# Optimization experiments

Measured on AMD Instinct MI355X. Metric: run time of the kernel, lower is better.

The kernel has to match this reference:

```python
import jax, jax.numpy as jnp
import numpy as np

HIDDEN = 512
BATCH = 32
SEQ = 4096


def setup_inputs() -> dict:
    key = jax.random.key(0)
    ks = jax.random.split(key, 8)
    s = 1.0 / np.sqrt(HIDDEN)
    return {
        "encoder_outputs": jax.random.normal(ks[0], (BATCH, SEQ, HIDDEN), jnp.float32),
        "decoder_hidden": jax.random.normal(ks[1], (BATCH, HIDDEN), jnp.float32),
        "W_enc": jax.random.uniform(ks[2], (HIDDEN, HIDDEN), jnp.float32, -s, s),
        "b_enc": jax.random.uniform(ks[3], (HIDDEN,), jnp.float32, -s, s),
        "W_dec": jax.random.uniform(ks[4], (HIDDEN, HIDDEN), jnp.float32, -s, s),
        "b_dec": jax.random.uniform(ks[5], (HIDDEN,), jnp.float32, -s, s),
        "W_v": jax.random.uniform(ks[6], (HIDDEN, 1), jnp.float32, -s, s),
        "b_v": jax.random.uniform(ks[7], (1,), jnp.float32, -s, s),
    }


def reference(encoder_outputs, decoder_hidden, W_enc, b_enc, W_dec, b_dec, W_v, b_v):
    # (b, s, h) projected encoder states
    enc_proj = jnp.einsum("bsh,hk->bsk", encoder_outputs, W_enc) + b_enc
    # (b, 1, h) projected decoder state, broadcast-added over seq
    dec_proj = (decoder_hidden @ W_dec + b_dec)[:, None, :]
    # score: (b, s, 1)
    score = jnp.tanh(enc_proj + dec_proj) @ W_v + b_v
    attention_weights = jax.nn.softmax(score, axis=1)  # softmax over seq_len
    # context: (b, h) weighted sum of encoder outputs
    context = jnp.sum(attention_weights * encoder_outputs, axis=1)
    return context, jnp.squeeze(attention_weights, -1)
```

## Files before the change

### kernel.cpp

```cpp
#include <hip/hip_runtime.h>
#include <hip/hip_bf16.h>

typedef __attribute__((ext_vector_type(8))) short bf16x8;
typedef __attribute__((ext_vector_type(4))) float f32x4;

#define HID 512
#define NB 32
#define SEQL 4096
#define BM 64
#define NKC 16
#define NBLK 2048
#define APAD 8
#define AW (HID + APAD)

#define WS_BP    0
#define WS_DPROJ (512*1024)
#define WS_SUM   (576*1024)

__device__ __forceinline__ short f2bf(float f) {
    unsigned u = __float_as_uint(f);
    unsigned r = (u + 0x7fffu + ((u >> 16) & 1u)) >> 16;
    return (short)r;
}

__device__ __forceinline__ float fast_tanh(float x) {
    float e = __expf(2.0f * x);
    float r = __builtin_amdgcn_rcpf(e + 1.0f);
    return 1.0f - 2.0f * r;
}

__global__ void k_pre(const float* __restrict__ We, short* __restrict__ Bp,
                      const float* __restrict__ dec, const float* __restrict__ Wd,
                      const float* __restrict__ be, const float* __restrict__ bd,
                      float* __restrict__ dproj, float* __restrict__ out,
                      float* __restrict__ sumacc) {
    const int blk = blockIdx.x, t = threadIdx.x;
    if (blk < 128) {
        int tid  = blk * 256 + t;
        int lane = tid & 63;
        int nt   = (tid >> 6) & 31;
        int kc   = tid >> 11;
        int k0   = kc * 32 + (lane >> 4) * 8;
        int n    = nt * 16 + (lane & 15);
        bf16x8 v;
#pragma unroll
        for (int j = 0; j < 8; ++j) v[j] = f2bf(We[(size_t)(k0 + j) * HID + n]);
        *(bf16x8*)&Bp[(size_t)tid * 8] = v;
    } else if (blk < 640) {
        __shared__ float red[8][33];
        int bid2 = blk - 128;
        int b  = bid2 >> 4, kg = bid2 & 15;
        int kl = t & 31,    hc = t >> 5;
        int k  = kg * 32 + kl;
        const float* dr = dec + (size_t)b * HID;
        float a = 0.f;
#pragma unroll 8
        for (int j = 0; j < 64; ++j) {
            int h = hc * 64 + j;
            a += dr[h] * Wd[(size_t)h * HID + k];
        }
        red[hc][kl] = a;
        __syncthreads();
        if (hc == 0) {
            float s = be[k] + bd[k];
#pragma unroll
            for (int c = 0; c < 8; ++c) s += red[c][kl];
            dproj[(size_t)b * HID + k] = s;
        }
    } else {
        int bz = blk - 640;
        out[bz * 256 + t] = 0.f;
        if (bz == 0 && t < NB) sumacc[t] = 0.f;
    }
}

__global__ __launch_bounds__(256, 2)
void k_main(const float* __restrict__ E, const short* __restrict__ Bp,
            const float* __restrict__ dproj, const float* __restrict__ Wv,
            float* __restrict__ out, float* __restrict__ sumacc) {
    __shared__ short As[BM][AW];
    __shared__ float fbuf[640];
    __shared__ float pbuf[BM];

    const int tid  = threadIdx.x;
    const int wave = tid >> 6, lane = tid & 63;
    const int quad = lane >> 4, l15 = lane & 15;
    const int bid  = blockIdx.x;
    const int row0 = bid * BM;
    const int b    = bid >> 6;

    f32x4 acc[4][8];
#pragma unroll
    for (int r = 0; r < 4; ++r)
#pragma unroll
        for (int c = 0; c < 8; ++c) acc[r][c] = (f32x4){0.f, 0.f, 0.f, 0.f};

    const float4* E4 = (const float4*)E + (size_t)row0 * (HID / 4);
    const int drow = tid >> 7;
    const int dcol = (tid & 127) * 4;
#pragma unroll
    for (int ph = 0; ph < 4; ++ph) {
        float4 v[8];
#pragma unroll
        for (int j = 0; j < 8; ++j)
            v[j] = E4[(size_t)(ph * 8 + j) * 256 + tid];
#pragma unroll
        for (int j = 0; j < 8; ++j) {
            int row = (ph * 8 + j) * 2 + drow;
            short4 s;
            s.x = f2bf(v[j].x); s.y = f2bf(v[j].y);
            s.z = f2bf(v[j].z); s.w = f2bf(v[j].w);
            *(short4*)&As[row][dcol] = s;
        }
    }

    const short* bbase = Bp + ((size_t)(wave * 8) * 64 + lane) * 8;
    bf16x8 fb[2][4][2];
    bf16x8 fbr[2][8];
#pragma unroll
    for (int c = 0; c < 8; ++c)
        fbr[0][c] = *(const bf16x8*)(bbase + (size_t)c * 64 * 8);

    __syncthreads();

    bf16x8 fa[2][4];
#pragma unroll
    for (int r = 0; r < 4; ++r)
        fa[0][r] = *(const bf16x8*)&As[r * 16 + l15][quad * 8];

#pragma unroll
    for (int kc = 0; kc < NKC; ++kc) {
        const int cur = kc & 1, nxt = cur ^ 1;
        if (kc + 1 < NKC) {
#pragma unroll
            for (int c = 0; c < 8; ++c)
                fbr[nxt][c] = *(const bf16x8*)(bbase + ((size_t)(kc + 1) * 2048 + c * 64) * 8);
#pragma unroll
            for (int r = 0; r < 4; ++r)
                fa[nxt][r] = *(const bf16x8*)&As[r * 16 + l15][(kc + 1) * 32 + quad * 8];
        }
#pragma unroll
        for (int c = 0; c < 8; ++c)
#pragma unroll
            for (int r = 0; r < 4; ++r)
                acc[r][c] = __builtin_amdgcn_mfma_f32_16x16x32_bf16(fa[cur][r], fbr[cur][c], acc[r][c], 0, 0, 0);
    }

    float part[4][4];
#pragma unroll
    for (int r = 0; r < 4; ++r)
#pragma unroll
        for (int g = 0; g < 4; ++g) part[r][g] = 0.f;
    const float* dp = dproj + (size_t)b * HID;
#pragma unroll
    for (int c = 0; c < 8; ++c) {
        int col = wave * 128 + c * 16 + l15;
        float dv = dp[col];
        float wv = Wv[col];
#pragma unroll
        for (int r = 0; r < 4; ++r)
#pragma unroll
            for (int g = 0; g < 4; ++g)
                part[r][g] += fast_tanh(acc[r][c][g] + dv) * wv;
    }
#pragma unroll
    for (int r = 0; r < 4; ++r)
#pragma unroll
        for (int g = 0; g < 4; ++g) {
            float v = part[r][g];
            v += __shfl_xor(v, 1); v += __shfl_xor(v, 2);
            v += __shfl_xor(v, 4); v += __shfl_xor(v, 8);
            part[r][g] = v;
        }
    if (l15 == 0) {
#pragma unroll
        for (int r = 0; r < 4; ++r)
#pragma unroll
            for (int g = 0; g < 4; ++g)
                fbuf[wave * 64 + r * 16 + quad * 4 + g] = part[r][g];
    }
    __syncthreads();
    if (tid < 64) {
        float s  = fbuf[tid] + fbuf[64 + tid] + fbuf[128 + tid] + fbuf[192 + tid];
        float pv = __expf(s);
        pbuf[tid] = pv;
        out[(size_t)NB * HID + row0 + tid] = pv;
        float t2 = pv;
        t2 += __shfl_xor(t2, 1);  t2 += __shfl_xor(t2, 2);  t2 += __shfl_xor(t2, 4);
        t2 += __shfl_xor(t2, 8);  t2 += __shfl_xor(t2, 16); t2 += __shfl_xor(t2, 32);
        if (tid == 0) atomicAdd(&sumacc[b], t2);
    }
    __syncthreads();

    const int hq = tid & 127, rh = tid >> 7;
    const float4* Eb = (const float4*)E;
    size_t cbase = (size_t)(row0 + rh * 32) * (HID / 4) + hq;
    float4 ca = {0.f, 0.f, 0.f, 0.f};
#pragma unroll 4
    for (int rr = 0; rr < 32; ++rr) {
        float w  = pbuf[rh * 32 + rr];
        float4 e = Eb[cbase + (size_t)rr * (HID / 4)];
        ca.x += w * e.x; ca.y += w * e.y; ca.z += w * e.z; ca.w += w * e.w;
    }
    if (rh == 1) {
        fbuf[hq] = ca.x; fbuf[128 + hq] = ca.y; fbuf[256 + hq] = ca.z; fbuf[384 + hq] = ca.w;
    }
    __syncthreads();
    if (rh == 0) {
        ca.x += fbuf[hq]; ca.y += fbuf[128 + hq]; ca.z += fbuf[256 + hq]; ca.w += fbuf[384 + hq];
        float* cg = out + (size_t)b * HID + hq * 4;
        atomicAdd(cg + 0, ca.x); atomicAdd(cg + 1, ca.y);
        atomicAdd(cg + 2, ca.z); atomicAdd(cg + 3, ca.w);
    }
}

__global__ void k_finish(float* __restrict__ out, const float* __restrict__ sumacc) {
    int b = blockIdx.x, t = threadIdx.x;
    float rs = 1.0f / sumacc[b];
    for (int i = t; i < HID; i += 256)
        out[(size_t)b * HID + i] *= rs;
    float* ow = out + (size_t)NB * HID + (size_t)b * SEQL;
    for (int i = t; i < SEQL; i += 256)
        ow[i] *= rs;
}

extern "C" void kernel_launch(void* const* d_in, const int* in_sizes, int n_in,
                              void* d_out, int out_size, void* d_ws, size_t ws_size,
                              hipStream_t stream) {
    const float* E   = (const float*)d_in[0];
    const float* dec = (const float*)d_in[1];
    const float* We  = (const float*)d_in[2];
    const float* be  = (const float*)d_in[3];
    const float* Wd  = (const float*)d_in[4];
    const float* bd  = (const float*)d_in[5];
    const float* Wv  = (const float*)d_in[6];
    float* out = (float*)d_out;
    char*  ws  = (char*)d_ws;
    short* Bp     = (short*)(ws + WS_BP);
    float* dproj  = (float*)(ws + WS_DPROJ);
    float* sumacc = (float*)(ws + WS_SUM);

    k_pre<<<704, 256, 0, stream>>>(We, Bp, dec, Wd, be, bd, dproj, out, sumacc);
    k_main<<<NBLK, 256, 0, stream>>>(E, Bp, dproj, Wv, out, sumacc);
    k_finish<<<NB, 256, 0, stream>>>(out, sumacc);
}
```

Measured before the change: 492.5 us.

## Give each wave its own 16 rows, drop LDS staging, and replace atomics with partial buffers

The main kernel now has each wave own 16 encoder rows. A operands are loaded straight from global memory into registers as bf16, with no LDS staging. The kernel loops over 32-column groups, streaming the B fragments from global memory/L2, and occupancy is raised to 4 blocks. Context and exp-sum partials are written per block to workspace, and the finish kernel reduces them in place of float atomics, so the zero-init pass goes away. The trade-off is that B-fragment reuse across rows drops: each wave re-reads all of W_enc, which adds L2 traffic in exchange for higher occupancy and no atomics.

```diff
diff --git a/kernel.cpp b/kernel.cpp
--- a/kernel.cpp
+++ b/kernel.cpp
@@ -7,15 +7,13 @@
 #define HID 512
 #define NB 32
 #define SEQL 4096
-#define BM 64
 #define NKC 16
 #define NBLK 2048
-#define APAD 8
-#define AW (HID + APAD)
 
 #define WS_BP    0
 #define WS_DPROJ (512*1024)
-#define WS_SUM   (576*1024)
+#define WS_PC    (576*1024)
+#define WS_PCS   (576*1024 + 4*1024*1024)
 
 __device__ __forceinline__ short f2bf(float f) {
     unsigned u = __float_as_uint(f);
@@ -32,8 +30,7 @@
 __global__ void k_pre(const float* __restrict__ We, short* __restrict__ Bp,
                       const float* __restrict__ dec, const float* __restrict__ Wd,
                       const float* __restrict__ be, const float* __restrict__ bd,
-                      float* __restrict__ dproj, float* __restrict__ out,
-                      float* __restrict__ sumacc) {
+                      float* __restrict__ dproj) {
     const int blk = blockIdx.x, t = threadIdx.x;
     if (blk < 128) {
         int tid  = blk * 256 + t;
@@ -46,7 +43,7 @@
 #pragma unroll
         for (int j = 0; j < 8; ++j) v[j] = f2bf(We[(size_t)(k0 + j) * HID + n]);
         *(bf16x8*)&Bp[(size_t)tid * 8] = v;
-    } else if (blk < 640) {
+    } else {
         __shared__ float red[8][33];
         int bid2 = blk - 128;
         int b  = bid2 >> 4, kg = bid2 & 15;
@@ -67,158 +64,135 @@
             for (int c = 0; c < 8; ++c) s += red[c][kl];
             dproj[(size_t)b * HID + k] = s;
         }
-    } else {
-        int bz = blk - 640;
-        out[bz * 256 + t] = 0.f;
-        if (bz == 0 && t < NB) sumacc[t] = 0.f;
-    }
-}
-
-__global__ __launch_bounds__(256, 2)
+    }
+}
+
+__global__ __launch_bounds__(256, 4)
 void k_main(const float* __restrict__ E, const short* __restrict__ Bp,
             const float* __restrict__ dproj, const float* __restrict__ Wv,
-            float* __restrict__ out, float* __restrict__ sumacc) {
-    __shared__ short As[BM][AW];
-    __shared__ float fbuf[640];
-    __shared__ float pbuf[BM];
+            float* __restrict__ outw, float* __restrict__ pc,
+            float* __restrict__ pcs) {
+    __shared__ float ctxs[4][HID];
+    __shared__ float ssum[4];
 
     const int tid  = threadIdx.x;
     const int wave = tid >> 6, lane = tid & 63;
     const int quad = lane >> 4, l15 = lane & 15;
     const int bid  = blockIdx.x;
-    const int row0 = bid * BM;
+    const int row0 = bid * 64 + wave * 16;
     const int b    = bid >> 6;
 
-    f32x4 acc[4][8];
-#pragma unroll
-    for (int r = 0; r < 4; ++r)
-#pragma unroll
-        for (int c = 0; c < 8; ++c) acc[r][c] = (f32x4){0.f, 0.f, 0.f, 0.f};
-
-    const float4* E4 = (const float4*)E + (size_t)row0 * (HID / 4);
-    const int drow = tid >> 7;
-    const int dcol = (tid & 127) * 4;
-#pragma unroll
-    for (int ph = 0; ph < 4; ++ph) {
-        float4 v[8];
-#pragma unroll
-        for (int j = 0; j < 8; ++j)
-            v[j] = E4[(size_t)(ph * 8 + j) * 256 + tid];
-#pragma unroll
-        for (int j = 0; j < 8; ++j) {
-            int row = (ph * 8 + j) * 2 + drow;
-            short4 s;
-            s.x = f2bf(v[j].x); s.y = f2bf(v[j].y);
-            s.z = f2bf(v[j].z); s.w = f2bf(v[j].w);
-            *(short4*)&As[row][dcol] = s;
-        }
-    }
-
-    const short* bbase = Bp + ((size_t)(wave * 8) * 64 + lane) * 8;
-    bf16x8 fb[2][4][2];
-    bf16x8 fbr[2][8];
-#pragma unroll
-    for (int c = 0; c < 8; ++c)
-        fbr[0][c] = *(const bf16x8*)(bbase + (size_t)c * 64 * 8);
-
+    const float* ap = E + (size_t)(row0 + l15) * HID + quad * 8;
+    bf16x8 fa[NKC];
+#pragma unroll
+    for (int kc = 0; kc < NKC; ++kc) {
+        float4 a0 = *(const float4*)(ap + kc * 32);
+        float4 a1 = *(const float4*)(ap + kc * 32 + 4);
+        bf16x8 v;
+        v[0] = f2bf(a0.x); v[1] = f2bf(a0.y); v[2] = f2bf(a0.z); v[3] = f2bf(a0.w);
+        v[4] = f2bf(a1.x); v[5] = f2bf(a1.y); v[6] = f2bf(a1.z); v[7] = f2bf(a1.w);
+        fa[kc] = v;
+    }
+
+    const short* bbl = Bp + (size_t)lane * 8;
+    const float* dp  = dproj + (size_t)b * HID;
+    float sp[4] = {0.f, 0.f, 0.f, 0.f};
+
+    for (int cg = 0; cg < 16; ++cg) {
+        f32x4 a0 = (f32x4){0.f, 0.f, 0.f, 0.f};
+        f32x4 a1 = (f32x4){0.f, 0.f, 0.f, 0.f};
+        const short* bcg = bbl + (size_t)(cg * 2) * 512;
+#pragma unroll
+        for (int kc = 0; kc < NKC; ++kc) {
+            bf16x8 fb0 = *(const bf16x8*)(bcg + (size_t)kc * 16384);
+            bf16x8 fb1 = *(const bf16x8*)(bcg + (size_t)kc * 16384 + 512);
+            a0 = __builtin_amdgcn_mfma_f32_16x16x32_bf16(fa[kc], fb0, a0, 0, 0, 0);
+            a1 = __builtin_amdgcn_mfma_f32_16x16x32_bf16(fa[kc], fb1, a1, 0, 0, 0);
+        }
+        int c0 = cg * 32 + l15;
+        float dv0 = dp[c0],      wv0 = Wv[c0];
+        float dv1 = dp[c0 + 16], wv1 = Wv[c0 + 16];
+#pragma unroll
+        for (int g = 0; g < 4; ++g) {
+            sp[g] += fast_tanh(a0[g] + dv0) * wv0;
+            sp[g] += fast_tanh(a1[g] + dv1) * wv1;
+        }
+    }
+
+#pragma unroll
+    for (int g = 0; g < 4; ++g) {
+        float v = sp[g];
+        v += __shfl_xor(v, 1); v += __shfl_xor(v, 2);
+        v += __shfl_xor(v, 4); v += __shfl_xor(v, 8);
+        sp[g] = v;
+    }
+    float pv[4];
+#pragma unroll
+    for (int g = 0; g < 4; ++g) pv[g] = __expf(sp[g]);
+    if (l15 == 0) {
+#pragma unroll
+        for (int g = 0; g < 4; ++g) outw[row0 + quad * 4 + g] = pv[g];
+    }
+    float ws = pv[0] + pv[1] + pv[2] + pv[3];
+    ws += __shfl_xor(ws, 16); ws += __shfl_xor(ws, 32);
+    if (lane == 0) ssum[wave] = ws;
+
+    float pvr[16];
+#pragma unroll
+    for (int r = 0; r < 16; ++r) pvr[r] = __shfl(pv[r & 3], (r >> 2) * 16);
+    const float* er = E + (size_t)row0 * HID + lane * 8;
+    f32x4 c0 = (f32x4){0.f, 0.f, 0.f, 0.f};
+    f32x4 c1 = (f32x4){0.f, 0.f, 0.f, 0.f};
+#pragma unroll
+    for (int r = 0; r < 16; ++r) {
+        float4 e0 = *(const float4*)(er + (size_t)r * HID);
+        float4 e1 = *(const float4*)(er + (size_t)r * HID + 4);
+        float w = pvr[r];
+        c0.x += w * e0.x; c0.y += w * e0.y; c0.z += w * e0.z; c0.w += w * e0.w;
+        c1.x += w * e1.x; c1.y += w * e1.y; c1.z += w * e1.z; c1.w += w * e1.w;
+    }
+    *(f32x4*)&ctxs[wave][lane * 8]     = c0;
+    *(f32x4*)&ctxs[wave][lane * 8 + 4] = c1;
     __syncthreads();
 
-    bf16x8 fa[2][4];
-#pragma unroll
-    for (int r = 0; r < 4; ++r)
-        fa[0][r] = *(const bf16x8*)&As[r * 16 + l15][quad * 8];
-
-#pragma unroll
-    for (int kc = 0; kc < NKC; ++kc) {
-        const int cur = kc & 1, nxt = cur ^ 1;
-        if (kc + 1 < NKC) {
-#pragma unroll
-            for (int c = 0; c < 8; ++c)
-                fbr[nxt][c] = *(const bf16x8*)(bbase + ((size_t)(kc + 1) * 2048 + c * 64) * 8);
-#pragma unroll
-            for (int r = 0; r < 4; ++r)
-                fa[nxt][r] = *(const bf16x8*)&As[r * 16 + l15][(kc + 1) * 32 + quad * 8];
-        }
-#pragma unroll
-        for (int c = 0; c < 8; ++c)
-#pragma unroll
-            for (int r = 0; r < 4; ++r)
-                acc[r][c] = __builtin_amdgcn_mfma_f32_16x16x32_bf16(fa[cur][r], fbr[cur][c], acc[r][c], 0, 0, 0);
-    }
-
-    float part[4][4];
-#pragma unroll
-    for (int r = 0; r < 4; ++r)
-#pragma unroll
-        for (int g = 0; g < 4; ++g) part[r][g] = 0.f;
-    const float* dp = dproj + (size_t)b * HID;
-#pragma unroll
-    for (int c = 0; c < 8; ++c) {
-        int col = wave * 128 + c * 16 + l15;
-        float dv = dp[col];
-        float wv = Wv[col];
-#pragma unroll
-        for (int r = 0; r < 4; ++r)
-#pragma unroll
-            for (int g = 0; g < 4; ++g)
-                part[r][g] += fast_tanh(acc[r][c][g] + dv) * wv;
-    }
-#pragma unroll
-    for (int r = 0; r < 4; ++r)
-#pragma unroll
-        for (int g = 0; g < 4; ++g) {
-            float v = part[r][g];
-            v += __shfl_xor(v, 1); v += __shfl_xor(v, 2);
-            v += __shfl_xor(v, 4); v += __shfl_xor(v, 8);
-            part[r][g] = v;
-        }
-    if (l15 == 0) {
-#pragma unroll
-        for (int r = 0; r < 4; ++r)
-#pragma unroll
-            for (int g = 0; g < 4; ++g)
-                fbuf[wave * 64 + r * 16 + quad * 4 + g] = part[r][g];
-    }
+    if (tid < 128) {
+        int h = tid * 4;
+        f32x4 s = *(f32x4*)&ctxs[0][h];
+        f32x4 s1 = *(f32x4*)&ctxs[1][h];
+        f32x4 s2 = *(f32x4*)&ctxs[2][h];
+        f32x4 s3 = *(f32x4*)&ctxs[3][h];
+        s.x += s1.x + s2.x + s3.x; s.y += s1.y + s2.y + s3.y;
+        s.z += s1.z + s2.z + s3.z; s.w += s1.w + s2.w + s3.w;
+        *(f32x4*)&pc[(size_t)bid * HID + h] = s;
+    }
+    if (tid == 0) pcs[bid] = ssum[0] + ssum[1] + ssum[2] + ssum[3];
+}
+
+__global__ void k_finish(float* __restrict__ out, const float* __restrict__ pc,
+                         const float* __restrict__ pcs) {
+    __shared__ float red[64];
+    const int b = blockIdx.x, t = threadIdx.x;
+    if (t < 64) red[t] = pcs[b * 64 + t];
     __syncthreads();
-    if (tid < 64) {
-        float s  = fbuf[tid] + fbuf[64 + tid] + fbuf[128 + tid] + fbuf[192 + tid];
-        float pv = __expf(s);
-        pbuf[tid] = pv;
-        out[(size_t)NB * HID + row0 + tid] = pv;
-        float t2 = pv;
-        t2 += __shfl_xor(t2, 1);  t2 += __shfl_xor(t2, 2);  t2 += __shfl_xor(t2, 4);
-        t2 += __shfl_xor(t2, 8);  t2 += __shfl_xor(t2, 16); t2 += __shfl_xor(t2, 32);
-        if (tid == 0) atomicAdd(&sumacc[b], t2);
+    if (t < 16) {
+        float s = red[t] + red[t + 16] + red[t + 32] + red[t + 48];
+        red[t] = s;
     }
     __syncthreads();
-
-    const int hq = tid & 127, rh = tid >> 7;
-    const float4* Eb = (const float4*)E;
-    size_t cbase = (size_t)(row0 + rh * 32) * (HID / 4) + hq;
-    float4 ca = {0.f, 0.f, 0.f, 0.f};
-#pragma unroll 4
-    for (int rr = 0; rr < 32; ++rr) {
-        float w  = pbuf[rh * 32 + rr];
-        float4 e = Eb[cbase + (size_t)rr * (HID / 4)];
-        ca.x += w * e.x; ca.y += w * e.y; ca.z += w * e.z; ca.w += w * e.w;
-    }
-    if (rh == 1) {
-        fbuf[hq] = ca.x; fbuf[128 + hq] = ca.y; fbuf[256 + hq] = ca.z; fbuf[384 + hq] = ca.w;
-    }
-    __syncthreads();
-    if (rh == 0) {
-        ca.x += fbuf[hq]; ca.y += fbuf[128 + hq]; ca.z += fbuf[256 + hq]; ca.w += fbuf[384 + hq];
-        float* cg = out + (size_t)b * HID + hq * 4;
-        atomicAdd(cg + 0, ca.x); atomicAdd(cg + 1, ca.y);
-        atomicAdd(cg + 2, ca.z); atomicAdd(cg + 3, ca.w);
-    }
-}
-
-__global__ void k_finish(float* __restrict__ out, const float* __restrict__ sumacc) {
-    int b = blockIdx.x, t = threadIdx.x;
-    float rs = 1.0f / sumacc[b];
-    for (int i = t; i < HID; i += 256)
-        out[(size_t)b * HID + i] *= rs;
+    float total = 0.f;
+#pragma unroll
+    for (int i = 0; i < 16; ++i) total += red[i];
+    float rs = 1.0f / total;
+
+    const float* pcb = pc + (size_t)b * 64 * HID;
+#pragma unroll
+    for (int hh = 0; hh < 2; ++hh) {
+        int h = t + hh * 256;
+        float a = 0.f;
+#pragma unroll 8
+        for (int w = 0; w < 64; ++w) a += pcb[(size_t)w * HID + h];
+        out[(size_t)b * HID + h] = a * rs;
+    }
     float* ow = out + (size_t)NB * HID + (size_t)b * SEQL;
     for (int i = t; i < SEQL; i += 256)
         ow[i] *= rs;
@@ -236,11 +210,13 @@
     const float* Wv  = (const float*)d_in[6];
     float* out = (float*)d_out;
     char*  ws  = (char*)d_ws;
-    short* Bp     = (short*)(ws + WS_BP);
-    float* dproj  = (float*)(ws + WS_DPROJ);
-    float* sumacc = (float*)(ws + WS_SUM);
-
-    k_pre<<<704, 256, 0, stream>>>(We, Bp, dec, Wd, be, bd, dproj, out, sumacc);
-    k_main<<<NBLK, 256, 0, stream>>>(E, Bp, dproj, Wv, out, sumacc);
-    k_finish<<<NB, 256, 0, stream>>>(out, sumacc);
-}
+    short* Bp    = (short*)(ws + WS_BP);
+    float* dproj = (float*)(ws + WS_DPROJ);
+    float* pc    = (float*)(ws + WS_PC);
+    float* pcs   = (float*)(ws + WS_PCS);
+    float* outw  = out + (size_t)NB * HID;
+
+    k_pre<<<640, 256, 0, stream>>>(We, Bp, dec, Wd, be, bd, dproj);
+    k_main<<<NBLK, 256, 0, stream>>>(E, Bp, dproj, Wv, outw, pc, pcs);
+    k_finish<<<NB, 256, 0, stream>>>(out, pc, pcs);
+}
```

New measurement: 572.4 us. +16.2%, slower.

## Halve row tile and chunk columns to cut registers and raise occupancy

Applied to the files above, without the earlier changes.

The main kernel now handles 32 sequence rows per block instead of 64, doubling the grid. The GEMM loop walks four column groups, each with a 2x2 accumulator tile, so the 128-register accumulator array shrinks to 16 registers; launch bounds ask for 4 blocks per CU. This should allow more waves to hide memory latency. In exchange, each block re-reads the full bf16 weight matrix over half as many rows, and the context stage issues twice as many atomics.

```diff
diff --git a/kernel.cpp b/kernel.cpp
--- a/kernel.cpp
+++ b/kernel.cpp
@@ -7,9 +7,9 @@
 #define HID 512
 #define NB 32
 #define SEQL 4096
-#define BM 64
 #define NKC 16
-#define NBLK 2048
+#define BMR 32
+#define NBLK 4096
 #define APAD 8
 #define AW (HID + APAD)
 
@@ -74,140 +74,130 @@
     }
 }
 
-__global__ __launch_bounds__(256, 2)
+__global__ __launch_bounds__(256, 4)
 void k_main(const float* __restrict__ E, const short* __restrict__ Bp,
             const float* __restrict__ dproj, const float* __restrict__ Wv,
             float* __restrict__ out, float* __restrict__ sumacc) {
-    __shared__ short As[BM][AW];
-    __shared__ float fbuf[640];
-    __shared__ float pbuf[BM];
+    __shared__ short As[BMR][AW];
+    __shared__ float sred[4][32];
+    __shared__ float pbuf[BMR];
+    __shared__ float cred[512];
 
     const int tid  = threadIdx.x;
     const int wave = tid >> 6, lane = tid & 63;
     const int quad = lane >> 4, l15 = lane & 15;
     const int bid  = blockIdx.x;
-    const int row0 = bid * BM;
-    const int b    = bid >> 6;
-
-    f32x4 acc[4][8];
-#pragma unroll
-    for (int r = 0; r < 4; ++r)
-#pragma unroll
-        for (int c = 0; c < 8; ++c) acc[r][c] = (f32x4){0.f, 0.f, 0.f, 0.f};
+    const int row0 = bid * BMR;
+    const int b    = bid >> 7;
 
     const float4* E4 = (const float4*)E + (size_t)row0 * (HID / 4);
-    const int drow = tid >> 7;
-    const int dcol = (tid & 127) * 4;
-#pragma unroll
-    for (int ph = 0; ph < 4; ++ph) {
-        float4 v[8];
-#pragma unroll
-        for (int j = 0; j < 8; ++j)
-            v[j] = E4[(size_t)(ph * 8 + j) * 256 + tid];
-#pragma unroll
-        for (int j = 0; j < 8; ++j) {
-            int row = (ph * 8 + j) * 2 + drow;
-            short4 s;
-            s.x = f2bf(v[j].x); s.y = f2bf(v[j].y);
-            s.z = f2bf(v[j].z); s.w = f2bf(v[j].w);
-            *(short4*)&As[row][dcol] = s;
-        }
-    }
-
-    const short* bbase = Bp + ((size_t)(wave * 8) * 64 + lane) * 8;
-    bf16x8 fb[2][4][2];
-    bf16x8 fbr[2][8];
-#pragma unroll
-    for (int c = 0; c < 8; ++c)
-        fbr[0][c] = *(const bf16x8*)(bbase + (size_t)c * 64 * 8);
-
-    __syncthreads();
-
-    bf16x8 fa[2][4];
-#pragma unroll
-    for (int r = 0; r < 4; ++r)
-        fa[0][r] = *(const bf16x8*)&As[r * 16 + l15][quad * 8];
-
-#pragma unroll
-    for (int kc = 0; kc < NKC; ++kc) {
-        const int cur = kc & 1, nxt = cur ^ 1;
-        if (kc + 1 < NKC) {
-#pragma unroll
-            for (int c = 0; c < 8; ++c)
-                fbr[nxt][c] = *(const bf16x8*)(bbase + ((size_t)(kc + 1) * 2048 + c * 64) * 8);
-#pragma unroll
-            for (int r = 0; r < 4; ++r)
-                fa[nxt][r] = *(const bf16x8*)&As[r * 16 + l15][(kc + 1) * 32 + quad * 8];
-        }
-#pragma unroll
-        for (int c = 0; c < 8; ++c)
-#pragma unroll
-            for (int r = 0; r < 4; ++r)
-                acc[r][c] = __builtin_amdgcn_mfma_f32_16x16x32_bf16(fa[cur][r], fbr[cur][c], acc[r][c], 0, 0, 0);
-    }
-
-    float part[4][4];
-#pragma unroll
-    for (int r = 0; r < 4; ++r)
-#pragma unroll
-        for (int g = 0; g < 4; ++g) part[r][g] = 0.f;
+#pragma unroll
+    for (int i = 0; i < 16; ++i) {
+        int f = i * 256 + tid;
+        float4 v = E4[f];
+        int row = f >> 7, c4 = f & 127;
+        short4 s;
+        s.x = f2bf(v.x); s.y = f2bf(v.y); s.z = f2bf(v.z); s.w = f2bf(v.w);
+        *(short4*)&As[row][c4 * 4] = s;
+    }
+    __syncthreads();
+
     const float* dp = dproj + (size_t)b * HID;
-#pragma unroll
-    for (int c = 0; c < 8; ++c) {
-        int col = wave * 128 + c * 16 + l15;
-        float dv = dp[col];
-        float wv = Wv[col];
-#pragma unroll
-        for (int r = 0; r < 4; ++r)
-#pragma unroll
-            for (int g = 0; g < 4; ++g)
-                part[r][g] += fast_tanh(acc[r][c][g] + dv) * wv;
-    }
-#pragma unroll
-    for (int r = 0; r < 4; ++r)
+    float sp[2][4] = {{0.f,0.f,0.f,0.f},{0.f,0.f,0.f,0.f}};
+
+#pragma unroll 1
+    for (int cg = 0; cg < 4; ++cg) {
+        const int ntb = wave * 8 + cg * 2;
+        const short* bcg = Bp + ((size_t)ntb * 64 + lane) * 8;
+        int col = wave * 128 + cg * 32 + l15;
+        float dv0 = dp[col],      wv0 = Wv[col];
+        float dv1 = dp[col + 16], wv1 = Wv[col + 16];
+
+        f32x4 acc[2][2];
+#pragma unroll
+        for (int rt = 0; rt < 2; ++rt)
+#pragma unroll
+            for (int ct = 0; ct < 2; ++ct) acc[rt][ct] = (f32x4){0.f,0.f,0.f,0.f};
+
+        bf16x8 cfb[2][2], cfa[2][2];
+        cfb[0][0] = *(const bf16x8*)(bcg);
+        cfb[0][1] = *(const bf16x8*)(bcg + 512);
+        cfa[0][0] = *(const bf16x8*)&As[l15][quad * 8];
+        cfa[0][1] = *(const bf16x8*)&As[16 + l15][quad * 8];
+#pragma unroll
+        for (int kc = 0; kc < NKC; ++kc) {
+            const int cur = kc & 1, nxt = cur ^ 1;
+            if (kc + 1 < NKC) {
+                const short* bn = bcg + (size_t)(kc + 1) * 16384;
+                cfb[nxt][0] = *(const bf16x8*)(bn);
+                cfb[nxt][1] = *(const bf16x8*)(bn + 512);
+                cfa[nxt][0] = *(const bf16x8*)&As[l15][(kc + 1) * 32 + quad * 8];
+                cfa[nxt][1] = *(const bf16x8*)&As[16 + l15][(kc + 1) * 32 + quad * 8];
+            }
+#pragma unroll
+            for (int rt = 0; rt < 2; ++rt)
+#pragma unroll
+                for (int ct = 0; ct < 2; ++ct)
+                    acc[rt][ct] = __builtin_amdgcn_mfma_f32_16x16x32_bf16(
+                        cfa[cur][rt], cfb[cur][ct], acc[rt][ct], 0, 0, 0);
+        }
+#pragma unroll
+        for (int rt = 0; rt < 2; ++rt)
+#pragma unroll
+            for (int g = 0; g < 4; ++g) {
+                sp[rt][g] += fast_tanh(acc[rt][0][g] + dv0) * wv0;
+                sp[rt][g] += fast_tanh(acc[rt][1][g] + dv1) * wv1;
+            }
+    }
+
+#pragma unroll
+    for (int rt = 0; rt < 2; ++rt)
 #pragma unroll
         for (int g = 0; g < 4; ++g) {
-            float v = part[r][g];
+            float v = sp[rt][g];
             v += __shfl_xor(v, 1); v += __shfl_xor(v, 2);
             v += __shfl_xor(v, 4); v += __shfl_xor(v, 8);
-            part[r][g] = v;
+            sp[rt][g] = v;
         }
     if (l15 == 0) {
 #pragma unroll
-        for (int r = 0; r < 4; ++r)
+        for (int rt = 0; rt < 2; ++rt)
 #pragma unroll
             for (int g = 0; g < 4; ++g)
-                fbuf[wave * 64 + r * 16 + quad * 4 + g] = part[r][g];
-    }
-    __syncthreads();
-    if (tid < 64) {
-        float s  = fbuf[tid] + fbuf[64 + tid] + fbuf[128 + tid] + fbuf[192 + tid];
+                sred[wave][rt * 16 + quad * 4 + g] = sp[rt][g];
+    }
+    __syncthreads();
+
+    if (tid < 32) {
+        float s = sred[0][tid] + sred[1][tid] + sred[2][tid] + sred[3][tid];
         float pv = __expf(s);
         pbuf[tid] = pv;
         out[(size_t)NB * HID + row0 + tid] = pv;
         float t2 = pv;
-        t2 += __shfl_xor(t2, 1);  t2 += __shfl_xor(t2, 2);  t2 += __shfl_xor(t2, 4);
-        t2 += __shfl_xor(t2, 8);  t2 += __shfl_xor(t2, 16); t2 += __shfl_xor(t2, 32);
+        t2 += __shfl_xor(t2, 1); t2 += __shfl_xor(t2, 2); t2 += __shfl_xor(t2, 4);
+        t2 += __shfl_xor(t2, 8); t2 += __shfl_xor(t2, 16);
         if (tid == 0) atomicAdd(&sumacc[b], t2);
     }
     __syncthreads();
 
     const int hq = tid & 127, rh = tid >> 7;
     const float4* Eb = (const float4*)E;
-    size_t cbase = (size_t)(row0 + rh * 32) * (HID / 4) + hq;
+    size_t cbase = (size_t)(row0 + rh * 16) * (HID / 4) + hq;
     float4 ca = {0.f, 0.f, 0.f, 0.f};
 #pragma unroll 4
-    for (int rr = 0; rr < 32; ++rr) {
-        float w  = pbuf[rh * 32 + rr];
+    for (int rr = 0; rr < 16; ++rr) {
+        float w  = pbuf[rh * 16 + rr];
         float4 e = Eb[cbase + (size_t)rr * (HID / 4)];
         ca.x += w * e.x; ca.y += w * e.y; ca.z += w * e.z; ca.w += w * e.w;
     }
     if (rh == 1) {
-        fbuf[hq] = ca.x; fbuf[128 + hq] = ca.y; fbuf[256 + hq] = ca.z; fbuf[384 + hq] = ca.w;
+        cred[hq] = ca.x; cred[128 + hq] = ca.y;
+        cred[256 + hq] = ca.z; cred[384 + hq] = ca.w;
     }
     __syncthreads();
     if (rh == 0) {
-        ca.x += fbuf[hq]; ca.y += fbuf[128 + hq]; ca.z += fbuf[256 + hq]; ca.w += fbuf[384 + hq];
+        ca.x += cred[hq]; ca.y += cred[128 + hq];
+        ca.z += cred[256 + hq]; ca.w += cred[384 + hq];
         float* cg = out + (size_t)b * HID + hq * 4;
         atomicAdd(cg + 0, ca.x); atomicAdd(cg + 1, ca.y);
         atomicAdd(cg + 2, ca.z); atomicAdd(cg + 3, ca.w);
```

New measurement: 648.5 us. 31.7% more time.
